# Kernel tuning notes

Measured on AMD Instinct MI355X. Metric: run time of the kernel, lower is better.

## Reference

```python
import jax, jax.numpy as jnp
import numpy as np

B, S, E, H, D = 2, 2048, 1024, 16, 64


def setup_inputs() -> dict:
    key = jax.random.key(0)
    ks = jax.random.split(key, 6)
    hidden_states = jax.random.normal(ks[0], (B, S, E), dtype=jnp.float32)
    # causal mask over (SeqLen, KeySeqLen): 1 = attend, 0 = blocked
    mask = jnp.tril(jnp.ones((S, S), dtype=jnp.float32))
    W_attn = jax.random.normal(ks[1], (E, 3, H, D), dtype=jnp.float32) * (E ** -0.5)
    b_attn = jnp.zeros((3, H, D), dtype=jnp.float32)
    W_proj = jax.random.normal(ks[2], (H, D, E), dtype=jnp.float32) * (E ** -0.5)
    b_proj = jnp.zeros((E,), dtype=jnp.float32)
    W_v_ff = jax.random.normal(ks[3], (E, E), dtype=jnp.float32) * (E ** -0.5)
    W_v_gate = jax.random.normal(ks[4], (E, E), dtype=jnp.float32) * (E ** -0.5)
    return {
        "hidden_states": hidden_states,
        "mask": mask,
        "layer_idx": 3,
        "W_attn": W_attn,
        "b_attn": b_attn,
        "W_proj": W_proj,
        "b_proj": b_proj,
        "W_v_ff": W_v_ff,
        "W_v_gate": W_v_gate,
    }


def reference(hidden_states, mask, layer_idx, W_attn, b_attn, W_proj, b_proj, W_v_ff, W_v_gate):
    dtype = hidden_states.dtype
    # c_attn: [B,S,E] -> [B,3,S,H,D]
    qkv = jnp.einsum("bse,eqhd->bqshd", hidden_states, W_attn) + b_attn[:, None, :, :]
    q, k, v = qkv[:, 0], qkv[:, 1], qkv[:, 2]  # [B,S,H,D] (k,v use key-seq axis)

    scale = jax.lax.rsqrt(float(D)) / (layer_idx + 1.0)  # scale_by_inverse_layer_idx
    q = q * scale
    # upcast to fp32 for score computation
    q32 = q.astype(jnp.float32)
    k32 = k.astype(jnp.float32)

    # attention scores: [B,H,S,Skv]
    scores = jnp.einsum("bshd,bthd->bhst", q32, k32)
    scores = scores + (1.0 - mask) * -1e9
    attn_weights = jax.nn.softmax(scores, axis=-1).astype(dtype)
    # dropout is identity (inference=True / p=0)

    # gated V FFN applied over the flattened (H,D) == Embed axis of v
    v_flat = v.reshape(B, S, E)
    v_gate = v_flat @ W_v_gate
    v_ff = v_flat @ W_v_ff
    v_gated = (jax.nn.relu(v_gate) * v_ff).reshape(B, S, H, D)

    # weighted sum over KeySeqLen: [B,S,H,D]
    attn_output = jnp.einsum("bhst,bthd->bshd", attn_weights, v_gated)
    # c_proj: [B,S,H,D] -> [B,S,E]
    out = jnp.einsum("bshd,hde->bse", attn_output, W_proj) + b_proj
    return out
```

## Files before the change

kernel.cpp:

```cpp
#include <hip/hip_runtime.h>
#include <hip/hip_bf16.h>
#include <cstdint>
#include <cstddef>

typedef unsigned short u16;
typedef __bf16 bf16x8 __attribute__((ext_vector_type(8)));
typedef float f32x4 __attribute__((ext_vector_type(4)));

#define LOG2E 1.44269504088896340736f

__device__ __forceinline__ uint32_t f2bf2(float lo, float hi) {
  uint32_t r;
  asm("v_cvt_pk_bf16_f32 %0, %1, %2" : "=v"(r) : "v"(lo), "v"(hi));
  return r;
}
__device__ __forceinline__ u16 f2bf(float f) { return (u16)f2bf2(f, f); }

__device__ __forceinline__ void gload16(const u16* g, u16* l) {
  __builtin_amdgcn_global_load_lds(
      (const __attribute__((address_space(1))) void*)g,
      (__attribute__((address_space(3))) void*)l, 16, 0, 0);
}

__global__ __launch_bounds__(256) void transpose_bf16_kernel(
    const float* __restrict__ src, u16* __restrict__ dst, int ld, int c0) {
  __shared__ u16 tile[64][65];
  const int r0 = blockIdx.x * 64, cl0 = blockIdx.y * 64;
  const int tid = threadIdx.x;
#pragma unroll
  for (int i = 0; i < 16; ++i) {
    int idx = i * 256 + tid;
    int r = idx >> 6, c = idx & 63;
    tile[c][r] = f2bf(src[(size_t)(r0 + r) * ld + c0 + cl0 + c]);
  }
  __syncthreads();
#pragma unroll
  for (int i = 0; i < 16; ++i) {
    int idx = i * 256 + tid;
    int c = idx >> 6, r = idx & 63;
    dst[(size_t)(cl0 + c) * 1024 + r0 + r] = tile[c][r];
  }
}

__global__ __launch_bounds__(256) void prep3_kernel(
    const float* __restrict__ Wa, const float* __restrict__ Wg,
    const float* __restrict__ Wf,
    u16* __restrict__ dv, u16* __restrict__ dg, u16* __restrict__ df) {
  __shared__ u16 tile[64][65];
  const int z = blockIdx.z;
  const float* src = (z == 0) ? Wa : (z == 1) ? Wg : Wf;
  u16* dst = (z == 0) ? dv : (z == 1) ? dg : df;
  const int ld = (z == 0) ? 3072 : 1024;
  const int c0 = (z == 0) ? 2048 : 0;
  const int r0 = blockIdx.x * 64, cl0 = blockIdx.y * 64;
  const int tid = threadIdx.x;
#pragma unroll
  for (int i = 0; i < 16; ++i) {
    int idx = i * 256 + tid;
    int r = idx >> 6, c = idx & 63;
    tile[c][r] = f2bf(src[(size_t)(r0 + r) * ld + c0 + cl0 + c]);
  }
  __syncthreads();
#pragma unroll
  for (int i = 0; i < 16; ++i) {
    int idx = i * 256 + tid;
    int c = idx >> 6, r = idx & 63;
    dst[(size_t)(cl0 + c) * 1024 + r0 + r] = tile[c][r];
  }
}

template <int EPI>
__global__ __launch_bounds__(256) void gemm_hA(
    const float* __restrict__ A,
    const u16* __restrict__ Bt,
    u16* __restrict__ O0, u16* __restrict__ O1,
    const float* __restrict__ bias,
    const int* __restrict__ layer_idx) {
  __shared__ u16 lds_a[2][64 * 40];
  __shared__ u16 lds_b[2][128 * 32];
  const int tid = threadIdx.x;
  const int wid = tid >> 6, lane = tid & 63;
  const int lrow = lane & 15, lgrp = lane >> 4;
  const int brow = blockIdx.y * 64;
  const int bcol = blockIdx.x * 128;
  const int wr = wid >> 1, wc = wid & 1;

  f32x4 acc[2][4] = {};

  const int wchunk0 = wid, wchunk1 = 4 + wid;
  const int cB0 = wchunk0 * 64 + lane, cB1 = wchunk1 * 64 + lane;
  const int rB0 = cB0 >> 2, col8B0 = (cB0 & 3) << 3;
  const int rB1 = cB1 >> 2, col8B1 = (cB1 & 3) << 3;

  gload16(Bt + (size_t)(bcol + rB0) * 1024 + col8B0, lds_b[0] + wchunk0 * 512);
  gload16(Bt + (size_t)(bcol + rB1) * 1024 + col8B1, lds_b[0] + wchunk1 * 512);
  {
    float4 v[2];
#pragma unroll
    for (int j = 0; j < 2; ++j) {
      int idx = j * 256 + tid;
      int m = idx >> 3, k4 = (idx & 7) << 2;
      v[j] = *(const float4*)(A + (size_t)(brow + m) * 1024 + k4);
    }
#pragma unroll
    for (int j = 0; j < 2; ++j) {
      int idx = j * 256 + tid;
      int m = idx >> 3, k4 = (idx & 7) << 2;
      uint2 w;
      w.x = f2bf2(v[j].x, v[j].y);
      w.y = f2bf2(v[j].z, v[j].w);
      *(uint2*)(lds_a[0] + m * 40 + k4) = w;
    }
  }

  for (int k0 = 0; k0 < 1024; k0 += 32) {
    const int bi = (k0 >> 5) & 1;
    __syncthreads();
    bf16x8 af[2], bfr[4];
#pragma unroll
    for (int mi = 0; mi < 2; ++mi)
      af[mi] = *(const bf16x8*)(lds_a[bi] + (wr * 32 + mi * 16 + lrow) * 40 + lgrp * 8);
#pragma unroll
    for (int nj = 0; nj < 4; ++nj)
      bfr[nj] = *(const bf16x8*)(lds_b[bi] + (wc * 64 + nj * 16 + lrow) * 32 + lgrp * 8);

    float4 v[2];
    if (k0 < 992) {
      const int kn = k0 + 32;
      gload16(Bt + (size_t)(bcol + rB0) * 1024 + kn + col8B0, lds_b[bi ^ 1] + wchunk0 * 512);
      gload16(Bt + (size_t)(bcol + rB1) * 1024 + kn + col8B1, lds_b[bi ^ 1] + wchunk1 * 512);
#pragma unroll
      for (int j = 0; j < 2; ++j) {
        int idx = j * 256 + tid;
        int m = idx >> 3, k4 = (idx & 7) << 2;
        v[j] = *(const float4*)(A + (size_t)(brow + m) * 1024 + kn + k4);
      }
    }

#pragma unroll
    for (int mi = 0; mi < 2; ++mi)
#pragma unroll
      for (int nj = 0; nj < 4; ++nj)
        acc[mi][nj] = __builtin_amdgcn_mfma_f32_16x16x32_bf16(af[mi], bfr[nj], acc[mi][nj], 0, 0, 0);

    if (k0 < 992) {
#pragma unroll
      for (int j = 0; j < 2; ++j) {
        int idx = j * 256 + tid;
        int m = idx >> 3, k4 = (idx & 7) << 2;
        uint2 w;
        w.x = f2bf2(v[j].x, v[j].y);
        w.y = f2bf2(v[j].z, v[j].w);
        *(uint2*)(lds_a[bi ^ 1] + m * 40 + k4) = w;
      }
    }
  }

  float scale = 1.0f;
  if (EPI == 0) scale = 0.125f * LOG2E / (1.0f + (float)(*layer_idx));

#pragma unroll
  for (int mi = 0; mi < 2; ++mi) {
#pragma unroll
    for (int nj = 0; nj < 4; ++nj) {
#pragma unroll
      for (int r = 0; r < 4; ++r) {
        int row = brow + wr * 32 + mi * 16 + lgrp * 4 + r;
        int col = bcol + wc * 64 + nj * 16 + lrow;
        float vv = acc[mi][nj][r] + bias[col];
        if (EPI == 0) {
          if (col < 1024) {
            O0[(size_t)row * 1024 + col] = f2bf(vv * scale);
          } else {
            O1[(size_t)row * 1024 + (col - 1024)] = f2bf(vv);
          }
        } else {
          size_t oidx = (size_t)(row >> 11) * 4194304 + (size_t)(row & 2047) * 1024 + col;
          O0[oidx] = f2bf(vv);
        }
      }
    }
  }
}

__global__ __launch_bounds__(256) void gemm_gate(
    const u16* __restrict__ A,
    const u16* __restrict__ Bg, const u16* __restrict__ Bf,
    u16* __restrict__ VgT) {
  __shared__ u16 lds_a[2][64 * 32];
  __shared__ u16 lds_g[2][128 * 32];
  __shared__ u16 lds_f[2][128 * 32];
  const int tid = threadIdx.x;
  const int wid = tid >> 6, lane = tid & 63;
  const int lrow = lane & 15, lgrp = lane >> 4;
  const int browg = blockIdx.y * 64;
  const int batch = browg >> 11;
  const int brow = browg & 2047;
  const u16* Ab = A + (size_t)batch * 4194304;
  u16* VgTb = VgT + (size_t)batch * 4194304;
  const int bcol = blockIdx.x * 128;
  const int wr = wid >> 1, wc = wid & 1;

  f32x4 accg[2][4] = {};
  f32x4 accf[2][4] = {};

  const int wchunk0 = wid, wchunk1 = 4 + wid;
  const int cA = wchunk0 * 64 + lane;
  const int rA = cA >> 2, col8A = (cA & 3) << 3;
  const int cB0 = wchunk0 * 64 + lane, cB1 = wchunk1 * 64 + lane;
  const int rB0 = cB0 >> 2, col8B0 = (cB0 & 3) << 3;
  const int rB1 = cB1 >> 2, col8B1 = (cB1 & 3) << 3;

  auto stage = [&](int k0, int bi) {
    gload16(Ab + (size_t)(brow + rA) * 1024 + k0 + col8A, lds_a[bi] + wchunk0 * 512);
    gload16(Bg + (size_t)(bcol + rB0) * 1024 + k0 + col8B0, lds_g[bi] + wchunk0 * 512);
    gload16(Bg + (size_t)(bcol + rB1) * 1024 + k0 + col8B1, lds_g[bi] + wchunk1 * 512);
    gload16(Bf + (size_t)(bcol + rB0) * 1024 + k0 + col8B0, lds_f[bi] + wchunk0 * 512);
    gload16(Bf + (size_t)(bcol + rB1) * 1024 + k0 + col8B1, lds_f[bi] + wchunk1 * 512);
  };

  stage(0, 0);
  for (int k0 = 0; k0 < 1024; k0 += 32) {
    const int bi = (k0 >> 5) & 1;
    __syncthreads();
    bf16x8 af[2], bg[4], bff[4];
#pragma unroll
    for (int mi = 0; mi < 2; ++mi)
      af[mi] = *(const bf16x8*)(lds_a[bi] + (wr * 32 + mi * 16 + lrow) * 32 + lgrp * 8);
#pragma unroll
    for (int nj = 0; nj < 4; ++nj) {
      bg[nj]  = *(const bf16x8*)(lds_g[bi] + (wc * 64 + nj * 16 + lrow) * 32 + lgrp * 8);
      bff[nj] = *(const bf16x8*)(lds_f[bi] + (wc * 64 + nj * 16 + lrow) * 32 + lgrp * 8);
    }
    if (k0 < 992) stage(k0 + 32, bi ^ 1);
#pragma unroll
    for (int mi = 0; mi < 2; ++mi)
#pragma unroll
      for (int nj = 0; nj < 4; ++nj) {
        accg[mi][nj] = __builtin_amdgcn_mfma_f32_16x16x32_bf16(af[mi], bg[nj],  accg[mi][nj], 0, 0, 0);
        accf[mi][nj] = __builtin_amdgcn_mfma_f32_16x16x32_bf16(af[mi], bff[nj], accf[mi][nj], 0, 0, 0);
      }
  }

#pragma unroll
  for (int mi = 0; mi < 2; ++mi) {
#pragma unroll
    for (int nj = 0; nj < 4; ++nj) {
      int row0 = brow + wr * 32 + mi * 16 + lgrp * 4;
      int n = bcol + wc * 64 + nj * 16 + lrow;
      uint2 w;
      w.x = f2bf2(fmaxf(accg[mi][nj][0], 0.f) * accf[mi][nj][0],
                  fmaxf(accg[mi][nj][1], 0.f) * accf[mi][nj][1]);
      w.y = f2bf2(fmaxf(accg[mi][nj][2], 0.f) * accf[mi][nj][2],
                  fmaxf(accg[mi][nj][3], 0.f) * accf[mi][nj][3]);
      *(uint2*)(VgTb + (size_t)n * 2048 + row0) = w;
    }
  }
}

__global__ __launch_bounds__(256) void gemm_projf(
    const u16* __restrict__ A,
    const float* __restrict__ Wp,
    float* __restrict__ Cout,
    const float* __restrict__ bias) {
  __shared__ u16 lds_a[2][64 * 32];
  __shared__ u16 lds_bt[2][64 * 40];
  const int tid = threadIdx.x;
  const int wid = tid >> 6, lane = tid & 63;
  const int lrow = lane & 15, lgrp = lane >> 4;
  const int brow = blockIdx.y * 64;
  const int bcol = blockIdx.x * 64;
  const int wr = wid >> 1, wc = wid & 1;

  f32x4 acc[2][2] = {};

  const int cA = wid * 64 + lane;
  const int rA = cA >> 2, col8A = (cA & 3) << 3;
  const int ng = tid & 15, kp = tid >> 4;
  const int n4 = ng << 2, kk = kp << 1;
  const int kc = kk >> 3, klo = kk & 7;

  auto stageB = [&](int k0, int bi) {
    float4 va = *(const float4*)(Wp + (size_t)(k0 + kk) * 1024 + bcol + n4);
    float4 vb = *(const float4*)(Wp + (size_t)(k0 + kk + 1) * 1024 + bcol + n4);
    const float a4[4] = {va.x, va.y, va.z, va.w};
    const float b4[4] = {vb.x, vb.y, vb.z, vb.w};
#pragma unroll
    for (int i = 0; i < 4; ++i) {
      int row = n4 + i;
      int sw = (kc ^ ((row >> 2) & 3)) << 3;
      u16* p = lds_bt[bi] + row * 40 + sw + klo;
      *(uint32_t*)p = f2bf2(a4[i], b4[i]);
    }
  };

  gload16(A + (size_t)(brow + rA) * 1024 + col8A, lds_a[0] + wid * 512);
  stageB(0, 0);

  for (int k0 = 0; k0 < 1024; k0 += 32) {
    const int bi = (k0 >> 5) & 1;
    __syncthreads();
    bf16x8 af[2], bfr[2];
#pragma unroll
    for (int mi = 0; mi < 2; ++mi)
      af[mi] = *(const bf16x8*)(lds_a[bi] + (wr * 32 + mi * 16 + lrow) * 32 + lgrp * 8);
#pragma unroll
    for (int nj = 0; nj < 2; ++nj) {
      int rowb = wc * 32 + nj * 16 + lrow;
      bfr[nj] = *(const bf16x8*)(lds_bt[bi] + rowb * 40 + ((lgrp ^ ((rowb >> 2) & 3)) << 3));
    }

    if (k0 < 992) {
      const int kn = k0 + 32;
      gload16(A + (size_t)(brow + rA) * 1024 + kn + col8A, lds_a[bi ^ 1] + wid * 512);
      stageB(kn, bi ^ 1);
    }

#pragma unroll
    for (int mi = 0; mi < 2; ++mi)
#pragma unroll
      for (int nj = 0; nj < 2; ++nj)
        acc[mi][nj] = __builtin_amdgcn_mfma_f32_16x16x32_bf16(af[mi], bfr[nj], acc[mi][nj], 0, 0, 0);
  }

#pragma unroll
  for (int mi = 0; mi < 2; ++mi)
#pragma unroll
    for (int nj = 0; nj < 2; ++nj)
#pragma unroll
      for (int r = 0; r < 4; ++r) {
        int row = brow + wr * 32 + mi * 16 + lgrp * 4 + r;
        int col = bcol + wc * 32 + nj * 16 + lrow;
        Cout[(size_t)row * 1024 + col] = acc[mi][nj][r] + bias[col];
      }
}

__global__ __launch_bounds__(256) void attn_kernel(
    const u16* Qb, const u16* __restrict__ Kb,
    const u16* __restrict__ VgTb, u16* AO) {
  __shared__ u16 lds_k[2][128 * 64];
  __shared__ u16 lds_v[2][64 * 128];
  __shared__ u16 lds_p[4][16 * 128];
  const int tid = threadIdx.x, wid = tid >> 6, lane = tid & 63;
  const int lrow = lane & 15, lgrp = lane >> 4;
  const int f = blockIdx.x;
  const int h = f & 15;
  const int idx = f >> 4;
  const int qt = (idx < 16) ? idx : 47 - idx;
  const int nt = (qt >> 1) + 1;

  bf16x8 qf[2];
  {
    const u16* qp = Qb + (size_t)(qt * 64 + wid * 16 + lrow) * 1024 + h * 64 + lgrp * 8;
    qf[0] = *(const bf16x8*)(qp);
    qf[1] = *(const bf16x8*)(qp + 32);
  }

  int krow[4], kch[4], vrow[4], vch[4];
#pragma unroll
  for (int i = 0; i < 4; ++i) {
    int c = i * 256 + tid;
    krow[i] = c >> 3; kch[i] = c & 7;
    vrow[i] = c >> 4; vch[i] = c & 15;
  }
  bf16x8 kreg[4], vreg[4];

  auto stage_load = [&](int t) {
#pragma unroll
    for (int i = 0; i < 4; ++i) {
      kreg[i] = *(const bf16x8*)(Kb + (size_t)(t * 128 + krow[i]) * 1024 + h * 64 + kch[i] * 8);
      vreg[i] = *(const bf16x8*)(VgTb + (size_t)(h * 64 + vrow[i]) * 2048 + t * 128 + vch[i] * 8);
    }
  };
  auto stage_write = [&](int bi) {
#pragma unroll
    for (int i = 0; i < 4; ++i) {
      *(bf16x8*)(lds_k[bi] + krow[i] * 64 + ((kch[i] ^ (krow[i] & 7)) << 3)) = kreg[i];
      *(bf16x8*)(lds_v[bi] + vrow[i] * 128 + ((vch[i] ^ (vrow[i] & 7)) << 3)) = vreg[i];
    }
  };

  stage_load(0);
  stage_write(0);
  __syncthreads();

  f32x4 oacc[4] = {};
  float lsum[4] = {0.f, 0.f, 0.f, 0.f};
  u16* pw = lds_p[wid];

  for (int t = 0; t < nt; ++t) {
    const int bi = t & 1;
    if (t + 1 < nt) stage_load(t + 1);

    f32x4 sacc[8] = {};
#pragma unroll
    for (int ks = 0; ks < 2; ++ks)
#pragma unroll
      for (int nj = 0; nj < 8; ++nj) {
        bf16x8 kf = *(const bf16x8*)(lds_k[bi] + (nj * 16 + lrow) * 64 + (((ks * 4 + lgrp) ^ (lrow & 7)) << 3));
        sacc[nj] = __builtin_amdgcn_mfma_f32_16x16x32_bf16(qf[ks], kf, sacc[nj], 0, 0, 0);
      }

    const bool last = (t == nt - 1);
#pragma unroll
    for (int nj = 0; nj < 8; ++nj) {
#pragma unroll
      for (int r = 0; r < 4; ++r) {
        const int srow = qt * 64 + wid * 16 + lgrp * 4 + r;
        float p;
        if (last && (t * 128 + nj * 16 + lrow > srow)) {
          p = 0.f;
        } else {
          p = exp2f(sacc[nj][r]);
        }
        lsum[r] += p;
        const int prow = lgrp * 4 + r;
        const int pch = (nj * 2 + (lrow >> 3)) ^ (prow & 7);
        pw[prow * 128 + (pch << 3) + (lrow & 7)] = f2bf(p);
      }
    }

#pragma unroll
    for (int ks = 0; ks < 4; ++ks) {
      bf16x8 pf = *(const bf16x8*)(pw + lrow * 128 + (((ks * 4 + lgrp) ^ (lrow & 7)) << 3));
#pragma unroll
      for (int nj = 0; nj < 4; ++nj) {
        bf16x8 vf = *(const bf16x8*)(lds_v[bi] + (nj * 16 + lrow) * 128 + (((ks * 4 + lgrp) ^ (lrow & 7)) << 3));
        oacc[nj] = __builtin_amdgcn_mfma_f32_16x16x32_bf16(pf, vf, oacc[nj], 0, 0, 0);
      }
    }

    if (t + 1 < nt) {
      stage_write(bi ^ 1);
      __syncthreads();
    }
  }

#pragma unroll
  for (int r = 0; r < 4; ++r) {
#pragma unroll
    for (int off = 1; off < 16; off <<= 1) lsum[r] += __shfl_xor(lsum[r], off);
    lsum[r] = 1.0f / lsum[r];
  }

#pragma unroll
  for (int nj = 0; nj < 4; ++nj) {
#pragma unroll
    for (int r = 0; r < 4; ++r) {
      const int srow = qt * 64 + wid * 16 + lgrp * 4 + r;
      AO[(size_t)srow * 1024 + h * 64 + nj * 16 + lrow] = f2bf(oacc[nj][r] * lsum[r]);
    }
  }
}

extern "C" void kernel_launch(void* const* d_in, const int* in_sizes, int n_in,
                              void* d_out, int out_size, void* d_ws, size_t ws_size,
                              hipStream_t stream) {
  const float* hidden    = (const float*)d_in[0];
  const int*   layer_idx = (const int*)d_in[2];
  const float* W_attn    = (const float*)d_in[3];
  const float* b_attn    = (const float*)d_in[4];
  const float* W_proj    = (const float*)d_in[5];
  const float* b_proj    = (const float*)d_in[6];
  const float* W_v_ff    = (const float*)d_in[7];
  const float* W_v_gate  = (const float*)d_in[8];

  const size_t MB = 1ull << 20;
  char* ob = (char*)d_out;
  u16* QA = (u16*)(ob);
  u16* QB = (u16*)(ob + 4 * MB);
  u16* QC = (u16*)(ob + 8 * MB);
  u16* QD = (u16*)(ob + 12 * MB);
  u16* WS  = (u16*)d_ws;
  u16* WfT = WS + 1024 * 1024;

  const float* hid0 = hidden;
  const float* hid1 = hidden + (size_t)2048 * 1024;

  prep3_kernel<<<dim3(16, 16, 3), 256, 0, stream>>>(W_attn, W_v_gate, W_v_ff, QD, WS, WfT);
  gemm_hA<1><<<dim3(8, 64), 256, 0, stream>>>(hidden, QD, QA, nullptr, b_attn + 2048, nullptr);
  gemm_gate<<<dim3(8, 64), 256, 0, stream>>>(QA, WS, WfT, QB);
  transpose_bf16_kernel<<<dim3(16, 32), 256, 0, stream>>>(W_attn, QC, 3072, 0);
  gemm_hA<0><<<dim3(16, 32), 256, 0, stream>>>(hid0, QC, WS, QA, b_attn, layer_idx);
  attn_kernel<<<512, 256, 0, stream>>>(WS, QA, QB, WS);
  gemm_hA<0><<<dim3(16, 32), 256, 0, stream>>>(hid1, QC, QA, QB, b_attn, layer_idx);
  attn_kernel<<<512, 256, 0, stream>>>(QA, QB, QD, QA);
  gemm_projf<<<dim3(16, 32), 256, 0, stream>>>(QA, W_proj, (float*)d_out + (size_t)2048 * 1024, b_proj);
  gemm_projf<<<dim3(16, 32), 256, 0, stream>>>(WS, W_proj, (float*)d_out, b_proj);
}
```

Measured before the change: 226.0 us.

## Split attention keys across waves and keep P in registers via transposed S

```diff
diff --git a/kernel.cpp b/kernel.cpp
--- a/kernel.cpp
+++ b/kernel.cpp
@@ -248,12 +248,15 @@
     for (int nj = 0; nj < 4; ++nj) {
       int row0 = brow + wr * 32 + mi * 16 + lgrp * 4;
       int n = bcol + wc * 64 + nj * 16 + lrow;
+      int k5 = row0 & 31;
+      int s0 = (k5 < 16) ? ((k5 >> 2) * 8) : (((k5 - 16) >> 2) * 8 + 4);
+      int pos = (row0 & ~31) + s0;
       uint2 w;
       w.x = f2bf2(fmaxf(accg[mi][nj][0], 0.f) * accf[mi][nj][0],
                   fmaxf(accg[mi][nj][1], 0.f) * accf[mi][nj][1]);
       w.y = f2bf2(fmaxf(accg[mi][nj][2], 0.f) * accf[mi][nj][2],
                   fmaxf(accg[mi][nj][3], 0.f) * accf[mi][nj][3]);
-      *(uint2*)(VgTb + (size_t)n * 2048 + row0) = w;
+      *(uint2*)(VgTb + (size_t)n * 2048 + pos) = w;
     }
   }
 }
@@ -338,9 +341,8 @@
 __global__ __launch_bounds__(256) void attn_kernel(
     const u16* Qb, const u16* __restrict__ Kb,
     const u16* __restrict__ VgTb, u16* AO) {
-  __shared__ u16 lds_k[2][128 * 64];
-  __shared__ u16 lds_v[2][64 * 128];
-  __shared__ u16 lds_p[4][16 * 128];
+  __shared__ u16 lds_kv[2][16384];
+  __shared__ float lds_ls[4][64];
   const int tid = threadIdx.x, wid = tid >> 6, lane = tid & 63;
   const int lrow = lane & 15, lgrp = lane >> 4;
   const int f = blockIdx.x;
@@ -349,11 +351,12 @@
   const int qt = (idx < 16) ? idx : 47 - idx;
   const int nt = (qt >> 1) + 1;
 
-  bf16x8 qf[2];
-  {
-    const u16* qp = Qb + (size_t)(qt * 64 + wid * 16 + lrow) * 1024 + h * 64 + lgrp * 8;
-    qf[0] = *(const bf16x8*)(qp);
-    qf[1] = *(const bf16x8*)(qp + 32);
+  bf16x8 qf[4][2];
+#pragma unroll
+  for (int qg = 0; qg < 4; ++qg) {
+    const u16* qp = Qb + (size_t)(qt * 64 + qg * 16 + lrow) * 1024 + h * 64 + lgrp * 8;
+    qf[qg][0] = *(const bf16x8*)(qp);
+    qf[qg][1] = *(const bf16x8*)(qp + 32);
   }
 
   int krow[4], kch[4], vrow[4], vch[4];
@@ -375,8 +378,8 @@
   auto stage_write = [&](int bi) {
 #pragma unroll
     for (int i = 0; i < 4; ++i) {
-      *(bf16x8*)(lds_k[bi] + krow[i] * 64 + ((kch[i] ^ (krow[i] & 7)) << 3)) = kreg[i];
-      *(bf16x8*)(lds_v[bi] + vrow[i] * 128 + ((vch[i] ^ (vrow[i] & 7)) << 3)) = vreg[i];
+      *(bf16x8*)(lds_kv[bi] + krow[i] * 64 + ((kch[i] ^ (krow[i] & 7)) << 3)) = kreg[i];
+      *(bf16x8*)(lds_kv[bi] + 8192 + vrow[i] * 128 + ((vch[i] ^ (vrow[i] & 7)) << 3)) = vreg[i];
     }
   };
 
@@ -384,71 +387,105 @@
   stage_write(0);
   __syncthreads();
 
-  f32x4 oacc[4] = {};
+  f32x4 oacc[4][4] = {};
   float lsum[4] = {0.f, 0.f, 0.f, 0.f};
-  u16* pw = lds_p[wid];
 
   for (int t = 0; t < nt; ++t) {
     const int bi = t & 1;
     if (t + 1 < nt) stage_load(t + 1);
-
-    f32x4 sacc[8] = {};
+    const u16* lk = lds_kv[bi];
+    const u16* lv = lds_kv[bi] + 8192;
+
+    bf16x8 kf[2][2];
 #pragma unroll
     for (int ks = 0; ks < 2; ++ks)
 #pragma unroll
-      for (int nj = 0; nj < 8; ++nj) {
-        bf16x8 kf = *(const bf16x8*)(lds_k[bi] + (nj * 16 + lrow) * 64 + (((ks * 4 + lgrp) ^ (lrow & 7)) << 3));
-        sacc[nj] = __builtin_amdgcn_mfma_f32_16x16x32_bf16(qf[ks], kf, sacc[nj], 0, 0, 0);
-      }
+      for (int nj2 = 0; nj2 < 2; ++nj2) {
+        int row = wid * 32 + nj2 * 16 + lrow;
+        kf[ks][nj2] = *(const bf16x8*)(lk + row * 64 + (((ks * 4 + lgrp) ^ (lrow & 7)) << 3));
+      }
+    bf16x8 vf[4];
+#pragma unroll
+    for (int dt = 0; dt < 4; ++dt)
+      vf[dt] = *(const bf16x8*)(lv + (dt * 16 + lrow) * 128 + (((wid * 4 + lgrp) ^ (lrow & 7)) << 3));
+
+    f32x4 sacc[4][2] = {};
+#pragma unroll
+    for (int qg = 0; qg < 4; ++qg)
+#pragma unroll
+      for (int ks = 0; ks < 2; ++ks)
+#pragma unroll
+        for (int nj2 = 0; nj2 < 2; ++nj2)
+          sacc[qg][nj2] = __builtin_amdgcn_mfma_f32_16x16x32_bf16(kf[ks][nj2], qf[qg][ks], sacc[qg][nj2], 0, 0, 0);
 
     const bool last = (t == nt - 1);
 #pragma unroll
-    for (int nj = 0; nj < 8; ++nj) {
-#pragma unroll
-      for (int r = 0; r < 4; ++r) {
-        const int srow = qt * 64 + wid * 16 + lgrp * 4 + r;
-        float p;
-        if (last && (t * 128 + nj * 16 + lrow > srow)) {
-          p = 0.f;
-        } else {
-          p = exp2f(sacc[nj][r]);
+    for (int qg = 0; qg < 4; ++qg) {
+#pragma unroll
+      for (int nj2 = 0; nj2 < 2; ++nj2) {
+#pragma unroll
+        for (int r = 0; r < 4; ++r) {
+          float p;
+          if (last) {
+            int key = t * 128 + wid * 32 + nj2 * 16 + lgrp * 4 + r;
+            int srow = qt * 64 + qg * 16 + lrow;
+            p = (key > srow) ? 0.f : exp2f(sacc[qg][nj2][r]);
+          } else {
+            p = exp2f(sacc[qg][nj2][r]);
+          }
+          sacc[qg][nj2][r] = p;
+          lsum[qg] += p;
         }
-        lsum[r] += p;
-        const int prow = lgrp * 4 + r;
-        const int pch = (nj * 2 + (lrow >> 3)) ^ (prow & 7);
-        pw[prow * 128 + (pch << 3) + (lrow & 7)] = f2bf(p);
-      }
-    }
-
-#pragma unroll
-    for (int ks = 0; ks < 4; ++ks) {
-      bf16x8 pf = *(const bf16x8*)(pw + lrow * 128 + (((ks * 4 + lgrp) ^ (lrow & 7)) << 3));
-#pragma unroll
-      for (int nj = 0; nj < 4; ++nj) {
-        bf16x8 vf = *(const bf16x8*)(lds_v[bi] + (nj * 16 + lrow) * 128 + (((ks * 4 + lgrp) ^ (lrow & 7)) << 3));
-        oacc[nj] = __builtin_amdgcn_mfma_f32_16x16x32_bf16(pf, vf, oacc[nj], 0, 0, 0);
-      }
-    }
-
-    if (t + 1 < nt) {
-      stage_write(bi ^ 1);
-      __syncthreads();
-    }
-  }
-
-#pragma unroll
-  for (int r = 0; r < 4; ++r) {
-#pragma unroll
-    for (int off = 1; off < 16; off <<= 1) lsum[r] += __shfl_xor(lsum[r], off);
-    lsum[r] = 1.0f / lsum[r];
-  }
-
-#pragma unroll
-  for (int nj = 0; nj < 4; ++nj) {
+      }
+    }
+
+#pragma unroll
+    for (int qg = 0; qg < 4; ++qg) {
+      union { uint32_t u[4]; bf16x8 v; } pa;
+      pa.u[0] = f2bf2(sacc[qg][0][0], sacc[qg][0][1]);
+      pa.u[1] = f2bf2(sacc[qg][0][2], sacc[qg][0][3]);
+      pa.u[2] = f2bf2(sacc[qg][1][0], sacc[qg][1][1]);
+      pa.u[3] = f2bf2(sacc[qg][1][2], sacc[qg][1][3]);
+#pragma unroll
+      for (int dt = 0; dt < 4; ++dt)
+        oacc[qg][dt] = __builtin_amdgcn_mfma_f32_16x16x32_bf16(pa.v, vf[dt], oacc[qg][dt], 0, 0, 0);
+    }
+
+    if (t + 1 < nt) stage_write(bi ^ 1);
+    __syncthreads();
+  }
+
+#pragma unroll
+  for (int qg = 0; qg < 4; ++qg) {
+    lsum[qg] += __shfl_xor(lsum[qg], 16);
+    lsum[qg] += __shfl_xor(lsum[qg], 32);
+  }
+  if (lgrp == 0) {
+#pragma unroll
+    for (int qg = 0; qg < 4; ++qg) lds_ls[wid][qg * 16 + lrow] = lsum[qg];
+  }
+
+  float* red = (float*)lds_kv;
+#pragma unroll
+  for (int qg = 0; qg < 4; ++qg)
+#pragma unroll
+    for (int dt = 0; dt < 4; ++dt)
+      *(f32x4*)(red + dt * 4096 + qg * 1024 + wid * 256 + lane * 4) = oacc[qg][dt];
+  __syncthreads();
+
+#pragma unroll
+  for (int qg = 0; qg < 4; ++qg) {
+    f32x4 s = *(const f32x4*)(red + wid * 4096 + qg * 1024 + 0 * 256 + lane * 4);
+#pragma unroll
+    for (int w = 1; w < 4; ++w) {
+      f32x4 x = *(const f32x4*)(red + wid * 4096 + qg * 1024 + w * 256 + lane * 4);
+      s[0] += x[0]; s[1] += x[1]; s[2] += x[2]; s[3] += x[3];
+    }
 #pragma unroll
     for (int r = 0; r < 4; ++r) {
-      const int srow = qt * 64 + wid * 16 + lgrp * 4 + r;
-      AO[(size_t)srow * 1024 + h * 64 + nj * 16 + lrow] = f2bf(oacc[nj][r] * lsum[r]);
+      int q = qg * 16 + lgrp * 4 + r;
+      float ls = lds_ls[0][q] + lds_ls[1][q] + lds_ls[2][q] + lds_ls[3][q];
+      AO[(size_t)(qt * 64 + q) * 1024 + h * 64 + wid * 16 + lrow] = f2bf(s[r] / ls);
     }
   }
 }
```

Result: faster. 217.4 us (-3.8%).
